# Kernel tuning notes

Measured on AMD Instinct MI355X. Metric: run time of the kernel, lower is better.

## Reference

```python
import jax, jax.numpy as jnp
import numpy as np

N, E, T = 8192, 131072, 12
H = 64        # node/edge/global hidden size
F = 1         # node_attr_size
OUT = 1       # out_size


def setup_inputs() -> dict:
    key = jax.random.key(0)
    ks = jax.random.split(key, 32)
    rn = lambda k, s, sc=1.0: jax.random.normal(k, s, dtype=jnp.float32) * sc
    w = 0.05  # weight scale
    inp = {
        "node_attrs": rn(ks[0], (T, N, F)),
        "edge_attrs": jax.random.uniform(ks[1], (T, E, 1), dtype=jnp.float32),
        "global_attr": rn(ks[2], (1, H)),
        "sp_L": rn(ks[3], (N, N), 0.01),
        "coeff": jax.random.uniform(ks[4], (1,), dtype=jnp.float32),
        # encoders
        "w_edge_enc": rn(ks[5], (H, 1), w), "b_edge_enc": jnp.zeros((H,), jnp.float32),
        "w_node_enc": rn(ks[6], (H, F), w), "b_node_enc": jnp.zeros((H,), jnp.float32),
        # block MLPs: in-dims from the Linear defs in __init__
        "w_eb": rn(ks[7], (H, (H + 2 * H) * 2 + H), w), "b_eb": jnp.zeros((H,), jnp.float32),
        "w_nb": rn(ks[8], (H, 2 * H + 2 * H + H), w), "b_nb": jnp.zeros((H,), jnp.float32),
        "w_gb": rn(ks[9], (H, H + H + H), w), "b_gb": jnp.zeros((H,), jnp.float32),
        # GRU (1 layer, input F, hidden H) + output head
        "gru_w_ih": rn(ks[10], (3 * H, F), w), "gru_w_hh": rn(ks[11], (3 * H, H), w),
        "gru_b_ih": jnp.zeros((3 * H,), jnp.float32), "gru_b_hh": jnp.zeros((3 * H,), jnp.float32),
        "w_lout": rn(ks[12], (OUT, H), w), "b_lout": jnp.zeros((OUT,), jnp.float32),
        "edge_index": jax.random.randint(ks[13], (2, E), 0, N),
        "num_processing_steps": T,
    }
    return inp


def _forward(node_attrs, edge_attrs, global_attr, sp_L, coeff,
             w_edge_enc, b_edge_enc, w_node_enc, b_node_enc,
             w_eb, b_eb, w_nb, b_nb, w_gb, b_gb,
             gru_w_ih, gru_w_hh, gru_b_ih, gru_b_hh,
             w_lout, b_lout, edge_index):
    n_nodes = node_attrs.shape[1]
    n_edges = edge_attrs.shape[1]
    send, recv = edge_index[0], edge_index[1]

    # encoders (edge_enc / node_enc), applied per time step
    enc_e = jax.nn.relu(jnp.einsum('tef,hf->teh', edge_attrs, w_edge_enc) + b_edge_enc)  # [T,E,H]
    enc_n = jax.nn.relu(jnp.einsum('tnf,hf->tnh', node_attrs, w_node_enc) + b_node_enc)  # [T,N,H]

    # per-node GRU over the T-step scalar history (torch nn.GRU math)
    def gru_step(h, x_t):  # h [N,H], x_t [N,F]
        gx = x_t @ gru_w_ih.T + gru_b_ih   # [N,3H]
        gh = h @ gru_w_hh.T + gru_b_hh     # [N,3H]
        xr, xz, xn = jnp.split(gx, 3, axis=-1)
        hr, hz, hn = jnp.split(gh, 3, axis=-1)
        r = jax.nn.sigmoid(xr + hr)
        z = jax.nn.sigmoid(xz + hz)
        n = jnp.tanh(xn + r * hn)
        return (1.0 - z) * n + z * h, None

    h0 = jnp.zeros((n_nodes, gru_w_hh.shape[1]), node_attrs.dtype)
    hT, _ = jax.lax.scan(gru_step, h0, node_attrs)          # [N,H]
    his = hT @ w_lout.T + b_lout                            # [N,OUT] == nodes_attr_based_on_his

    # GN layer 1: recurrent hidden graph (h_init zeros), per-step edge/node/global blocks
    def gn_step(carry, xs):
        hx, he, gl = carry          # hidden node [N,H], hidden edge [E,H], global [1,H]
        nx, ee = xs                 # encoded node [N,H], encoded edge [E,H]
        gl_e = jnp.broadcast_to(gl, (n_edges, gl.shape[1]))
        e_in = jnp.concatenate([ee, nx[send], nx[recv], he, hx[send], hx[recv], gl_e], axis=-1)
        new_e = jax.nn.relu(e_in @ w_eb.T + b_eb)           # [E,H]
        sent = jax.ops.segment_sum(new_e, send, num_segments=n_nodes)   # scatter_add by sender
        recvd = jax.ops.segment_sum(new_e, recv, num_segments=n_nodes)  # scatter_add by receiver
        gl_n = jnp.broadcast_to(gl, (n_nodes, gl.shape[1]))
        n_in = jnp.concatenate([nx, hx, recvd, sent, gl_n], axis=-1)
        new_n = jax.nn.relu(n_in @ w_nb.T + b_nb)           # [N,H]
        g_in = jnp.concatenate([new_n.mean(0, keepdims=True),
                                new_e.mean(0, keepdims=True), gl], axis=-1)
        new_g = jax.nn.relu(g_in @ w_gb.T + b_gb)           # [1,H]
        sd = coeff[0] * (sp_L @ new_n)                      # spatial derivative (pde='diff')
        td = new_n - hx                                     # time derivative of hidden state
        return (new_n, new_e, new_g), (td, sd)

    hx0 = jnp.zeros_like(enc_n[0])
    he0 = jnp.zeros_like(enc_e[0])
    _, (tds, sds) = jax.lax.scan(gn_step, (hx0, he0, global_attr), (enc_n, enc_e))

    pred_result = his[None]  # skip=True path: pred = nodes_attr_based_on_his.unsqueeze(0)
    return pred_result, tds, sds


def reference(node_attrs, edge_attrs, global_attr, sp_L, coeff,
              w_edge_enc, b_edge_enc, w_node_enc, b_node_enc,
              w_eb, b_eb, w_nb, b_nb, w_gb, b_gb,
              gru_w_ih, gru_w_hh, gru_b_ih, gru_b_hh,
              w_lout, b_lout, edge_index, num_processing_steps):
    del num_processing_steps  # fixed to leading dim of node_attrs
    return _forward(node_attrs, edge_attrs, global_attr, sp_L, coeff,
                    w_edge_enc, b_edge_enc, w_node_enc, b_node_enc,
                    w_eb, b_eb, w_nb, b_nb, w_gb, b_gb,
                    gru_w_ih, gru_w_hh, gru_b_ih, gru_b_hh,
                    w_lout, b_lout, edge_index)
```

## Files before the change

### kernel.cpp

```cpp
#include <hip/hip_runtime.h>
#include <math.h>

#define NN 8192
#define NE 131072
#define TT 12

typedef __attribute__((ext_vector_type(8))) short bf16x8;
typedef __attribute__((ext_vector_type(4))) float f32x4;

static const size_t OFF_HX    = 0;
static const size_t OFF_HE0   = OFF_HX    + (size_t)NN*64;
static const size_t OFF_HE1   = OFF_HE0   + (size_t)NE*64;
static const size_t OFF_A25   = OFF_HE1   + (size_t)NE*64;
static const size_t OFF_A36   = OFF_A25   + (size_t)NN*64;
static const size_t OFF_SENT  = OFF_A36   + (size_t)NN*64;
static const size_t OFF_RECVD = OFF_SENT  + (size_t)NN*64;
static const size_t OFF_NEWN  = OFF_RECVD + (size_t)NN*64;
static const size_t OFF_GL    = OFF_NEWN  + (size_t)NN*TT*32;
static const size_t OFF_CBE   = OFF_GL    + 64;
static const size_t OFF_CBN   = OFF_CBE   + 64;
static const size_t OFF_ESUM  = OFF_CBN   + 64;
static const size_t OFF_NSUM  = OFF_ESUM  + 64;
static const size_t OFF_EBF   = OFF_NSUM  + 64;

__device__ inline unsigned short f2bf(float x) {
  union { float f; unsigned u; } v; v.f = x;
  unsigned r = v.u + 0x7fffu + ((v.u >> 16) & 1u);
  return (unsigned short)(r >> 16);
}
__device__ inline float bf2f(unsigned short h) {
  union { unsigned u; float f; } v; v.u = ((unsigned)h) << 16;
  return v.f;
}
__device__ inline void split8(const float* x, bf16x8& hi, bf16x8& lo) {
  #pragma unroll
  for (int j = 0; j < 8; ++j) {
    unsigned short h = f2bf(x[j]);
    hi[j] = (short)h;
    lo[j] = (short)f2bf(x[j] - bf2f(h));
  }
}

__global__ void init_kernel(float* __restrict__ ws, const float* __restrict__ global_attr) {
  size_t total = (size_t)NN*64 + (size_t)NE*64;
  for (size_t i = (size_t)blockIdx.x*blockDim.x + threadIdx.x; i < total;
       i += (size_t)gridDim.x*blockDim.x)
    ws[OFF_HX + i] = 0.f;
  if (blockIdx.x == 0 && threadIdx.x < 64)
    ws[OFF_GL + threadIdx.x] = global_attr[threadIdx.x];
}

__global__ void prep_kernel(const float* __restrict__ w_eb, const float* __restrict__ b_eb,
                            const float* __restrict__ w_nb, const float* __restrict__ b_nb,
                            float* __restrict__ ws) {
  int h = threadIdx.x;
  float se = b_eb[h], sn = b_nb[h];
  for (int c = 0; c < 64; ++c) {
    float g = ws[OFF_GL + c];
    se += w_eb[h*448 + 384 + c] * g;
    sn += w_nb[h*320 + 256 + c] * g;
  }
  ws[OFF_CBE + h] = se;
  ws[OFF_CBN + h] = sn;
  ws[OFF_ESUM + h] = 0.f;
  ws[OFF_NSUM + h] = 0.f;
}

__global__ void ebfrag_kernel(const float* __restrict__ w_eb, unsigned short* __restrict__ ebf) {
  int idx = blockIdx.x*256 + threadIdx.x;
  if (idx >= 24576) return;
  int s = idx >> 12;
  int rem = idx & 4095;
  int k = rem >> 6;
  int n = rem & 63;
  float w = (s < 3) ? w_eb[n*448 + k] : w_eb[n*448 + 192 + k];
  unsigned short h = f2bf(w);
  unsigned short l = f2bf(w - bf2f(h));
  unsigned short val = (s == 2 || s == 5) ? l : h;
  int kh = k >> 5, q = (k >> 3) & 3, j = k & 7;
  int nt = n >> 4, col = n & 15;
  int lane = q*16 + col;
  ebf[(((size_t)(s*2 + kh)*4 + nt)*64 + lane)*8 + j] = val;
}

__global__ __launch_bounds__(256) void gru_his_kernel(
    const float* __restrict__ node_attrs, const float* __restrict__ w_ih,
    const float* __restrict__ w_hh, const float* __restrict__ b_ih,
    const float* __restrict__ b_hh, const float* __restrict__ w_lout,
    const float* __restrict__ b_lout, float* __restrict__ pred_out)
{
  __shared__ float Whh[192*65];
  __shared__ float wih_s[192], bih_s[192], bhh_s[192], wlo_s[64];
  int tid = threadIdx.x;
  for (int i = tid; i < 192*64; i += 256) {
    int rr = i >> 6, k = i & 63;
    Whh[rr*65 + k] = w_hh[i];
  }
  for (int i = tid; i < 192; i += 256) { wih_s[i] = w_ih[i]; bih_s[i] = b_ih[i]; bhh_s[i] = b_hh[i]; }
  if (tid < 64) wlo_s[tid] = w_lout[tid];
  __syncthreads();
  int lane = tid & 63, wv = tid >> 6;
  int n = blockIdx.x*4 + wv;
  int j = lane;
  float h = 0.f;
  for (int t = 0; t < TT; ++t) {
    float x = node_attrs[t*NN + n];
    float ar = 0.f, az = 0.f, an = 0.f;
    #pragma unroll 16
    for (int k = 0; k < 64; ++k) {
      float hk = __shfl(h, k);
      ar += hk * Whh[j*65 + k];
      az += hk * Whh[(64+j)*65 + k];
      an += hk * Whh[(128+j)*65 + k];
    }
    float xr = x*wih_s[j]      + bih_s[j];
    float xz = x*wih_s[64+j]   + bih_s[64+j];
    float xn = x*wih_s[128+j]  + bih_s[128+j];
    float r  = 1.f/(1.f + expf(-(xr + ar + bhh_s[j])));
    float z  = 1.f/(1.f + expf(-(xz + az + bhh_s[64+j])));
    float nnv = tanhf(xn + r*(an + bhh_s[128+j]));
    h = (1.f - z)*nnv + z*h;
  }
  float v = h * wlo_s[j];
  #pragma unroll
  for (int off = 32; off >= 1; off >>= 1) v += __shfl_xor(v, off);
  if (lane == 0) pred_out[n] = v + b_lout[0];
}

__global__ __launch_bounds__(256) void node_proj_kernel(
    const float* __restrict__ node_attrs, const float* __restrict__ w_eb,
    const float* __restrict__ w_node_enc, const float* __restrict__ b_node_enc,
    float* __restrict__ ws, int t)
{
  __shared__ float W2[64*65], W3[64*65], W5[64*65], W6[64*65];
  __shared__ float wne[64], bne[64];
  int tid = threadIdx.x;
  for (int i = tid; i < 64*64; i += 256) {
    int h = i >> 6, c = i & 63;
    W2[h*65+c] = w_eb[h*448 + 64  + c];
    W3[h*65+c] = w_eb[h*448 + 128 + c];
    W5[h*65+c] = w_eb[h*448 + 256 + c];
    W6[h*65+c] = w_eb[h*448 + 320 + c];
  }
  if (tid < 64) { wne[tid] = w_node_enc[tid]; bne[tid] = b_node_enc[tid]; }
  __syncthreads();
  int lane = tid & 63, wv = tid >> 6;
  float* A25 = ws + OFF_A25; float* A36 = ws + OFF_A36;
  float* hx = ws + OFF_HX;
  float* sent = ws + OFF_SENT; float* recvd = ws + OFF_RECVD;
  for (int q = 0; q < 4; ++q) {
    int n = blockIdx.x*16 + wv*4 + q;
    float na = node_attrs[t*NN + n];
    float nx = fmaxf(na*wne[lane] + bne[lane], 0.f);
    float hv = hx[n*64 + lane];
    float a2 = 0.f, a3 = 0.f, a5 = 0.f, a6 = 0.f;
    #pragma unroll 16
    for (int c = 0; c < 64; ++c) {
      float nxc = __shfl(nx, c);
      float hvc = __shfl(hv, c);
      int wi = lane*65 + c;
      a2 += W2[wi]*nxc; a3 += W3[wi]*nxc;
      a5 += W5[wi]*hvc; a6 += W6[wi]*hvc;
    }
    A25[n*64+lane] = a2 + a5; A36[n*64+lane] = a3 + a6;
    sent[n*64+lane] = 0.f; recvd[n*64+lane] = 0.f;
  }
}

__global__ __launch_bounds__(256) void edge_mfma_kernel(
    const float* __restrict__ edge_attrs, const int* __restrict__ edge_index,
    const float* __restrict__ w_edge_enc, const float* __restrict__ b_edge_enc,
    const unsigned short* __restrict__ ebf, float* __restrict__ ws,
    const float* __restrict__ he_cur, float* __restrict__ he_next, int t)
{
  __shared__ unsigned short Bs[12*4*64*8];
  __shared__ float wee_s[64], bee_s[64], cbe_s[64];
  __shared__ float esum_s[64];
  int tid = threadIdx.x;
  for (int i = tid; i < 3072; i += 256)
    ((uint4*)Bs)[i] = ((const uint4*)ebf)[i];
  if (tid < 64) { wee_s[tid]=w_edge_enc[tid]; bee_s[tid]=b_edge_enc[tid]; cbe_s[tid]=ws[OFF_CBE+tid]; esum_s[tid]=0.f; }
  __syncthreads();
  int lane = tid & 63, wv = tid >> 6;
  int m = lane & 15, q = lane >> 4;
  int e0 = blockIdx.x * 64;
  int em = e0 + wv*16 + m;
  float ea = edge_attrs[(size_t)t*NE + em];
  bf16x8 eeH[2], eeL[2], heH[2], heL[2];
  #pragma unroll
  for (int kh = 0; kh < 2; ++kh) {
    float xs[8];
    #pragma unroll
    for (int j = 0; j < 8; ++j) {
      int c = kh*32 + q*8 + j;
      xs[j] = fmaxf(ea*wee_s[c] + bee_s[c], 0.f);
    }
    split8(xs, eeH[kh], eeL[kh]);
    float4 h0 = *(const float4*)(he_cur + (size_t)em*64 + kh*32 + q*8);
    float4 h1 = *(const float4*)(he_cur + (size_t)em*64 + kh*32 + q*8 + 4);
    float hs[8] = {h0.x,h0.y,h0.z,h0.w,h1.x,h1.y,h1.z,h1.w};
    split8(hs, heH[kh], heL[kh]);
  }
  f32x4 acc[4] = {};
  #pragma unroll
  for (int s = 0; s < 6; ++s) {
    #pragma unroll
    for (int kh = 0; kh < 2; ++kh) {
      bf16x8 a = (s==0||s==2) ? eeH[kh] : (s==1) ? eeL[kh] : (s==4) ? heL[kh] : heH[kh];
      const bf16x8* bp = (const bf16x8*)(Bs + (size_t)((s*2+kh)*4*64)*8);
      #pragma unroll
      for (int nt = 0; nt < 4; ++nt) {
        bf16x8 b = bp[nt*64 + lane];
        acc[nt] = __builtin_amdgcn_mfma_f32_16x16x32_bf16(a, b, acc[nt], 0, 0, 0);
      }
    }
  }
  const int* sendi = edge_index;
  const int* recvi = edge_index + NE;
  const float* A25 = ws + OFF_A25;
  const float* A36 = ws + OFF_A36;
  float* sent = ws + OFF_SENT; float* recvd = ws + OFF_RECVD;
  int col = lane & 15;
  float part[4] = {0.f, 0.f, 0.f, 0.f};
  #pragma unroll
  for (int r = 0; r < 4; ++r) {
    int e = e0 + wv*16 + q*4 + r;
    int se = sendi[e], re = recvi[e];
    #pragma unroll
    for (int nt = 0; nt < 4; ++nt) {
      int h = nt*16 + col;
      float v = acc[nt][r] + A25[(size_t)se*64 + h] + A36[(size_t)re*64 + h] + cbe_s[h];
      v = fmaxf(v, 0.f);
      he_next[(size_t)e*64 + h] = v;
      atomicAdd(&sent[(size_t)se*64 + h], v);
      atomicAdd(&recvd[(size_t)re*64 + h], v);
      part[nt] += v;
    }
  }
  #pragma unroll
  for (int nt = 0; nt < 4; ++nt) {
    part[nt] += __shfl_xor(part[nt], 16);
    part[nt] += __shfl_xor(part[nt], 32);
  }
  if (q == 0) {
    #pragma unroll
    for (int nt = 0; nt < 4; ++nt)
      atomicAdd(&esum_s[nt*16 + col], part[nt]);
  }
  __syncthreads();
  if (tid < 64) atomicAdd(&ws[OFF_ESUM + tid], esum_s[tid]);
}

__global__ __launch_bounds__(256) void node_kernel(
    const float* __restrict__ node_attrs, const float* __restrict__ w_nb,
    const float* __restrict__ w_node_enc, const float* __restrict__ b_node_enc,
    float* __restrict__ ws, float* __restrict__ tds_out, int t)
{
  __shared__ float B1[64*65], B2[64*65], B3[64*65], B4[64*65];
  __shared__ float wne[64], bne[64], cbn[64];
  __shared__ float nsum_s[4][64];
  int tid = threadIdx.x;
  for (int i = tid; i < 64*64; i += 256) {
    int h = i >> 6, c = i & 63;
    B1[h*65+c] = w_nb[h*320 + c];
    B2[h*65+c] = w_nb[h*320 + 64  + c];
    B3[h*65+c] = w_nb[h*320 + 128 + c];
    B4[h*65+c] = w_nb[h*320 + 192 + c];
  }
  if (tid < 64) { wne[tid] = w_node_enc[tid]; bne[tid] = b_node_enc[tid]; cbn[tid] = ws[OFF_CBN + tid]; }
  __syncthreads();
  int lane = tid & 63, wv = tid >> 6;
  float* hx = ws + OFF_HX;
  const float* sent = ws + OFF_SENT; const float* recvd = ws + OFF_RECVD;
  unsigned short* newnT = (unsigned short*)(ws + OFF_NEWN);
  float npart = 0.f;
  for (int q = 0; q < 4; ++q) {
    int n = blockIdx.x*16 + wv*4 + q;
    float na = node_attrs[t*NN + n];
    float nx = fmaxf(na*wne[lane] + bne[lane], 0.f);
    float hv = hx[n*64 + lane];
    float rc = recvd[n*64 + lane];
    float st = sent[n*64 + lane];
    float acc = 0.f;
    #pragma unroll 16
    for (int c = 0; c < 64; ++c) {
      float nxc = __shfl(nx, c);
      float hvc = __shfl(hv, c);
      float rcc = __shfl(rc, c);
      float stc = __shfl(st, c);
      int wi = lane*65 + c;
      acc += B1[wi]*nxc + B2[wi]*hvc + B3[wi]*rcc + B4[wi]*stc;
    }
    acc += cbn[lane];
    float nn = fmaxf(acc, 0.f);
    tds_out[(size_t)t*NN*64 + (size_t)n*64 + lane] = nn - hv;
    hx[n*64 + lane] = nn;
    newnT[(size_t)(t*64 + lane)*NN + n] = f2bf(nn);
    npart += nn;
  }
  nsum_s[wv][lane] = npart;
  __syncthreads();
  if (tid < 64)
    atomicAdd(&ws[OFF_NSUM + tid],
              nsum_s[0][tid] + nsum_s[1][tid] + nsum_s[2][tid] + nsum_s[3][tid]);
}

__global__ void global_prep_kernel(
    const float* __restrict__ w_gb, const float* __restrict__ b_gb,
    const float* __restrict__ w_eb, const float* __restrict__ b_eb,
    const float* __restrict__ w_nb, const float* __restrict__ b_nb,
    float* __restrict__ ws)
{
  int h = threadIdx.x;
  __shared__ float gin[192];
  __shared__ float gs[64];
  gin[h]       = ws[OFF_NSUM + h] * (1.0f/NN);
  gin[64 + h]  = ws[OFF_ESUM + h] * (1.0f/NE);
  gin[128 + h] = ws[OFF_GL + h];
  __syncthreads();
  float a = b_gb[h];
  for (int c = 0; c < 192; ++c) a += w_gb[h*192 + c] * gin[c];
  float g = fmaxf(a, 0.f);
  gs[h] = g;
  __syncthreads();
  ws[OFF_GL + h] = g;
  float se = b_eb[h], sn = b_nb[h];
  for (int c = 0; c < 64; ++c) {
    float gc = gs[c];
    se += w_eb[h*448 + 384 + c] * gc;
    sn += w_nb[h*320 + 256 + c] * gc;
  }
  ws[OFF_CBE + h] = se;
  ws[OFF_CBN + h] = sn;
  ws[OFF_ESUM + h] = 0.f;
  ws[OFF_NSUM + h] = 0.f;
}

__global__ __launch_bounds__(512) void sds_mfma_kernel(
    const float* __restrict__ A, const unsigned short* __restrict__ Bt,
    float* __restrict__ P0, float* __restrict__ P1)
{
  __shared__ unsigned short Asm[2][64][72];
  int tid = threadIdx.x;
  int lane = tid & 63, wv = tid >> 6;
  int q = lane >> 4, l16 = lane & 15;
  int m0 = blockIdx.y * 64;
  int kbase = blockIdx.x * (NN/2);
  float* P = (blockIdx.x == 0) ? P0 : P1;

  int sr = tid >> 3;
  int sc = (tid & 7) * 8;
  const float* ap = A + (size_t)(m0 + sr)*NN + kbase + sc;

  const unsigned short* bp[6];
  #pragma unroll
  for (int ni = 0; ni < 6; ++ni)
    bp[ni] = Bt + (size_t)(wv*96 + ni*16 + l16)*NN + kbase + q*8;

  f32x4 acc[4][6] = {};

  {
    float4 a0 = *(const float4*)ap;
    float4 a1 = *(const float4*)(ap + 4);
    float xs[8] = {a0.x,a0.y,a0.z,a0.w,a1.x,a1.y,a1.z,a1.w};
    bf16x8 w;
    #pragma unroll
    for (int j = 0; j < 8; ++j) w[j] = (short)f2bf(xs[j]);
    *(bf16x8*)&Asm[0][sr][sc] = w;
  }

  const int NSLICE = (NN/2)/64;
  for (int ks = 0; ks < NSLICE; ++ks) {
    int buf = ks & 1;
    float4 a0, a1;
    if (ks + 1 < NSLICE) {
      a0 = *(const float4*)(ap + (ks+1)*64);
      a1 = *(const float4*)(ap + (ks+1)*64 + 4);
    }
    __syncthreads();
    #pragma unroll
    for (int sub = 0; sub < 2; ++sub) {
      bf16x8 bfr[6];
      #pragma unroll
      for (int ni = 0; ni < 6; ++ni)
        bfr[ni] = *(const bf16x8*)(bp[ni] + ks*64 + sub*32);
      bf16x8 af[4];
      #pragma unroll
      for (int mi = 0; mi < 4; ++mi)
        af[mi] = *(const bf16x8*)&Asm[buf][mi*16 + l16][sub*32 + q*8];
      #pragma unroll
      for (int mi = 0; mi < 4; ++mi)
        #pragma unroll
        for (int ni = 0; ni < 6; ++ni)
          acc[mi][ni] = __builtin_amdgcn_mfma_f32_16x16x32_bf16(af[mi], bfr[ni], acc[mi][ni], 0, 0, 0);
    }
    __syncthreads();
    if (ks + 1 < NSLICE) {
      float xs[8] = {a0.x,a0.y,a0.z,a0.w,a1.x,a1.y,a1.z,a1.w};
      bf16x8 w;
      #pragma unroll
      for (int j = 0; j < 8; ++j) w[j] = (short)f2bf(xs[j]);
      *(bf16x8*)&Asm[1-buf][sr][sc] = w;
    }
  }

  #pragma unroll
  for (int mi = 0; mi < 4; ++mi) {
    int row = m0 + mi*16 + q*4;
    #pragma unroll
    for (int ni = 0; ni < 6; ++ni) {
      int cn = wv*96 + ni*16 + l16;
      int tt = cn >> 6, h = cn & 63;
      #pragma unroll
      for (int r = 0; r < 4; ++r)
        P[(size_t)tt*NN*64 + (size_t)(row + r)*64 + h] = acc[mi][ni][r];
    }
  }
}

__global__ __launch_bounds__(256) void sds_combine_kernel(
    const float* __restrict__ P0, const float* __restrict__ P1,
    float* __restrict__ C, const float* __restrict__ coeff)
{
  float cf = coeff[0];
  size_t total = (size_t)TT*NN*64/4;
  for (size_t i = (size_t)blockIdx.x*blockDim.x + threadIdx.x; i < total;
       i += (size_t)gridDim.x*blockDim.x) {
    float4 p0 = ((const float4*)P0)[i];
    float4 p1 = ((const float4*)P1)[i];
    float4 c;
    c.x = cf*(p0.x + p1.x); c.y = cf*(p0.y + p1.y);
    c.z = cf*(p0.z + p1.z); c.w = cf*(p0.w + p1.w);
    ((float4*)C)[i] = c;
  }
}

extern "C" void kernel_launch(void* const* d_in, const int* in_sizes, int n_in,
                              void* d_out, int out_size, void* d_ws, size_t ws_size,
                              hipStream_t stream) {
  const float* node_attrs  = (const float*)d_in[0];
  const float* edge_attrs  = (const float*)d_in[1];
  const float* global_attr = (const float*)d_in[2];
  const float* sp_L        = (const float*)d_in[3];
  const float* coeff       = (const float*)d_in[4];
  const float* w_edge_enc  = (const float*)d_in[5];
  const float* b_edge_enc  = (const float*)d_in[6];
  const float* w_node_enc  = (const float*)d_in[7];
  const float* b_node_enc  = (const float*)d_in[8];
  const float* w_eb        = (const float*)d_in[9];
  const float* b_eb        = (const float*)d_in[10];
  const float* w_nb        = (const float*)d_in[11];
  const float* b_nb        = (const float*)d_in[12];
  const float* w_gb        = (const float*)d_in[13];
  const float* b_gb        = (const float*)d_in[14];
  const float* gru_w_ih    = (const float*)d_in[15];
  const float* gru_w_hh    = (const float*)d_in[16];
  const float* gru_b_ih    = (const float*)d_in[17];
  const float* gru_b_hh    = (const float*)d_in[18];
  const float* w_lout      = (const float*)d_in[19];
  const float* b_lout      = (const float*)d_in[20];
  const int*   edge_index  = (const int*)d_in[21];

  float* ws  = (float*)d_ws;
  float* out = (float*)d_out;
  float* pred_out = out;
  float* tds_out  = out + NN;
  float* sds_out  = tds_out + (size_t)TT*NN*64;
  unsigned short* ebf = (unsigned short*)(ws + OFF_EBF);

  hipLaunchKernelGGL(init_kernel, dim3(1024), dim3(256), 0, stream, ws, global_attr);
  hipLaunchKernelGGL(ebfrag_kernel, dim3(96), dim3(256), 0, stream, w_eb, ebf);
  hipLaunchKernelGGL(gru_his_kernel, dim3(NN/4), dim3(256), 0, stream,
                     node_attrs, gru_w_ih, gru_w_hh, gru_b_ih, gru_b_hh,
                     w_lout, b_lout, pred_out);
  hipLaunchKernelGGL(prep_kernel, dim3(1), dim3(64), 0, stream, w_eb, b_eb, w_nb, b_nb, ws);

  for (int t = 0; t < TT; ++t) {
    float* he_cur  = ws + ((t & 1) ? OFF_HE1 : OFF_HE0);
    float* he_next = ws + ((t & 1) ? OFF_HE0 : OFF_HE1);
    hipLaunchKernelGGL(node_proj_kernel, dim3(NN/16), dim3(256), 0, stream,
                       node_attrs, w_eb, w_node_enc, b_node_enc, ws, t);
    hipLaunchKernelGGL(edge_mfma_kernel, dim3(NE/64), dim3(256), 0, stream,
                       edge_attrs, edge_index, w_edge_enc, b_edge_enc,
                       ebf, ws, he_cur, he_next, t);
    hipLaunchKernelGGL(node_kernel, dim3(NN/16), dim3(256), 0, stream,
                       node_attrs, w_nb, w_node_enc, b_node_enc, ws, tds_out, t);
    hipLaunchKernelGGL(global_prep_kernel, dim3(1), dim3(64), 0, stream,
                       w_gb, b_gb, w_eb, b_eb, w_nb, b_nb, ws);
  }

  hipLaunchKernelGGL(sds_mfma_kernel, dim3(2, NN/64), dim3(512), 0, stream,
                     sp_L, (const unsigned short*)(ws + OFF_NEWN),
                     ws + OFF_HE0, ws + OFF_HE1);
  hipLaunchKernelGGL(sds_combine_kernel, dim3(1536), dim3(256), 0, stream,
                     ws + OFF_HE0, ws + OFF_HE1, sds_out, coeff);
}
```

Measured before the change: 2.923 ms.

## Replace atomic scatter of edge messages with CSR gather in node kernel

Builds sender and receiver CSR indices once per call (histogram, scan, fill), then drops the per-edge float atomicAdds into sent/recvd. The node kernel now gathers the edge hidden states of each node's incident edges directly from he_next. This removes 2*E*64 atomics per step and the zeroing of the accumulators, at the cost of irregular gathers in the node kernel, extra setup kernels, and a single-block scan. Summation order also changes, so floating-point results are no longer order-nondeterministic but differ slightly from before.

Result: faster. 2.509 ms (-14.2%).

```diff
diff --git a/kernel.cpp b/kernel.cpp
--- a/kernel.cpp
+++ b/kernel.cpp
@@ -13,15 +13,15 @@
 static const size_t OFF_HE1   = OFF_HE0   + (size_t)NE*64;
 static const size_t OFF_A25   = OFF_HE1   + (size_t)NE*64;
 static const size_t OFF_A36   = OFF_A25   + (size_t)NN*64;
-static const size_t OFF_SENT  = OFF_A36   + (size_t)NN*64;
-static const size_t OFF_RECVD = OFF_SENT  + (size_t)NN*64;
-static const size_t OFF_NEWN  = OFF_RECVD + (size_t)NN*64;
+static const size_t OFF_CSR   = OFF_A36   + (size_t)NN*64;
+static const size_t OFF_NEWN  = OFF_CSR   + (size_t)2*NN*64;
 static const size_t OFF_GL    = OFF_NEWN  + (size_t)NN*TT*32;
 static const size_t OFF_CBE   = OFF_GL    + 64;
 static const size_t OFF_CBN   = OFF_CBE   + 64;
 static const size_t OFF_ESUM  = OFF_CBN   + 64;
 static const size_t OFF_NSUM  = OFF_ESUM  + 64;
 static const size_t OFF_EBF   = OFF_NSUM  + 64;
+
 
 __device__ inline unsigned short f2bf(float x) {
   union { float f; unsigned u; } v; v.f = x;
@@ -64,6 +64,69 @@
   ws[OFF_CBN + h] = sn;
   ws[OFF_ESUM + h] = 0.f;
   ws[OFF_NSUM + h] = 0.f;
+}
+
+__global__ void csr_zero_kernel(int* __restrict__ ibase) {
+  int* cnt = ibase + 2*(NN+1);
+  int i = blockIdx.x*256 + threadIdx.x;
+  if (i < 2*NN) cnt[i] = 0;
+}
+
+__global__ void csr_hist_kernel(const int* __restrict__ ei, int* __restrict__ ibase) {
+  int* cnt_s = ibase + 2*(NN+1);
+  int* cnt_r = cnt_s + NN;
+  int e = blockIdx.x*256 + threadIdx.x;
+  if (e < NE) {
+    atomicAdd(&cnt_s[ei[e]], 1);
+    atomicAdd(&cnt_r[ei[NE + e]], 1);
+  }
+}
+
+__global__ __launch_bounds__(256) void csr_scan_kernel(int* __restrict__ ibase) {
+  __shared__ int part[257];
+  int tid = threadIdx.x;
+  int* ptr_s = ibase;
+  int* ptr_r = ibase + (NN+1);
+  int* cnt_s = ibase + 2*(NN+1);
+  int* cnt_r = cnt_s + NN;
+  for (int a = 0; a < 2; ++a) {
+    int* cnt = a ? cnt_r : cnt_s;
+    int* ptr = a ? ptr_r : ptr_s;
+    int loc[32];
+    int base = tid*32;
+    int s = 0;
+    #pragma unroll
+    for (int i = 0; i < 32; ++i) { loc[i] = s; s += cnt[base + i]; }
+    part[tid] = s;
+    __syncthreads();
+    if (tid == 0) {
+      int acc = 0;
+      for (int i = 0; i < 256; ++i) { int t = part[i]; part[i] = acc; acc += t; }
+      part[256] = acc;
+    }
+    __syncthreads();
+    int off = part[tid];
+    #pragma unroll
+    for (int i = 0; i < 32; ++i) {
+      int v = off + loc[i];
+      ptr[base + i] = v;
+      cnt[base + i] = v;
+    }
+    if (tid == 0) ptr[NN] = part[256];
+    __syncthreads();
+  }
+}
+
+__global__ void csr_fill_kernel(const int* __restrict__ ei, int* __restrict__ ibase) {
+  int* cnt_s = ibase + 2*(NN+1);
+  int* cnt_r = cnt_s + NN;
+  int* csr_s = cnt_r + NN;
+  int* csr_r = csr_s + NE;
+  int e = blockIdx.x*256 + threadIdx.x;
+  if (e < NE) {
+    int p = atomicAdd(&cnt_s[ei[e]], 1);      csr_s[p] = e;
+    int q = atomicAdd(&cnt_r[ei[NE + e]], 1); csr_r[q] = e;
+  }
 }
 
 __global__ void ebfrag_kernel(const float* __restrict__ w_eb, unsigned short* __restrict__ ebf) {
@@ -147,7 +210,6 @@
   int lane = tid & 63, wv = tid >> 6;
   float* A25 = ws + OFF_A25; float* A36 = ws + OFF_A36;
   float* hx = ws + OFF_HX;
-  float* sent = ws + OFF_SENT; float* recvd = ws + OFF_RECVD;
   for (int q = 0; q < 4; ++q) {
     int n = blockIdx.x*16 + wv*4 + q;
     float na = node_attrs[t*NN + n];
@@ -163,7 +225,6 @@
       a5 += W5[wi]*hvc; a6 += W6[wi]*hvc;
     }
     A25[n*64+lane] = a2 + a5; A36[n*64+lane] = a3 + a6;
-    sent[n*64+lane] = 0.f; recvd[n*64+lane] = 0.f;
   }
 }
 
@@ -219,7 +280,6 @@
   const int* recvi = edge_index + NE;
   const float* A25 = ws + OFF_A25;
   const float* A36 = ws + OFF_A36;
-  float* sent = ws + OFF_SENT; float* recvd = ws + OFF_RECVD;
   int col = lane & 15;
   float part[4] = {0.f, 0.f, 0.f, 0.f};
   #pragma unroll
@@ -232,8 +292,6 @@
       float v = acc[nt][r] + A25[(size_t)se*64 + h] + A36[(size_t)re*64 + h] + cbe_s[h];
       v = fmaxf(v, 0.f);
       he_next[(size_t)e*64 + h] = v;
-      atomicAdd(&sent[(size_t)se*64 + h], v);
-      atomicAdd(&recvd[(size_t)re*64 + h], v);
       part[nt] += v;
     }
   }
@@ -254,7 +312,8 @@
 __global__ __launch_bounds__(256) void node_kernel(
     const float* __restrict__ node_attrs, const float* __restrict__ w_nb,
     const float* __restrict__ w_node_enc, const float* __restrict__ b_node_enc,
-    float* __restrict__ ws, float* __restrict__ tds_out, int t)
+    float* __restrict__ ws, float* __restrict__ tds_out,
+    const float* __restrict__ he, int t)
 {
   __shared__ float B1[64*65], B2[64*65], B3[64*65], B4[64*65];
   __shared__ float wne[64], bne[64], cbn[64];
@@ -271,16 +330,40 @@
   __syncthreads();
   int lane = tid & 63, wv = tid >> 6;
   float* hx = ws + OFF_HX;
-  const float* sent = ws + OFF_SENT; const float* recvd = ws + OFF_RECVD;
+  const int* ibase = (const int*)(ws + OFF_CSR);
+  const int* ptr_s = ibase;
+  const int* ptr_r = ibase + (NN+1);
+  const int* csr_s = ibase + 2*(NN+1) + 2*NN;
+  const int* csr_r = csr_s + NE;
   unsigned short* newnT = (unsigned short*)(ws + OFF_NEWN);
   float npart = 0.f;
   for (int q = 0; q < 4; ++q) {
     int n = blockIdx.x*16 + wv*4 + q;
+    float st = 0.f;
+    {
+      int i = ptr_s[n], end = ptr_s[n+1];
+      for (; i + 4 <= end; i += 4) {
+        int e0 = csr_s[i], e1 = csr_s[i+1], e2 = csr_s[i+2], e3 = csr_s[i+3];
+        float v0 = he[(size_t)e0*64 + lane], v1 = he[(size_t)e1*64 + lane];
+        float v2 = he[(size_t)e2*64 + lane], v3 = he[(size_t)e3*64 + lane];
+        st += (v0 + v1) + (v2 + v3);
+      }
+      for (; i < end; ++i) st += he[(size_t)csr_s[i]*64 + lane];
+    }
+    float rc = 0.f;
+    {
+      int i = ptr_r[n], end = ptr_r[n+1];
+      for (; i + 4 <= end; i += 4) {
+        int e0 = csr_r[i], e1 = csr_r[i+1], e2 = csr_r[i+2], e3 = csr_r[i+3];
+        float v0 = he[(size_t)e0*64 + lane], v1 = he[(size_t)e1*64 + lane];
+        float v2 = he[(size_t)e2*64 + lane], v3 = he[(size_t)e3*64 + lane];
+        rc += (v0 + v1) + (v2 + v3);
+      }
+      for (; i < end; ++i) rc += he[(size_t)csr_r[i]*64 + lane];
+    }
     float na = node_attrs[t*NN + n];
     float nx = fmaxf(na*wne[lane] + bne[lane], 0.f);
     float hv = hx[n*64 + lane];
-    float rc = recvd[n*64 + lane];
-    float st = sent[n*64 + lane];
     float acc = 0.f;
     #pragma unroll 16
     for (int c = 0; c < 64; ++c) {
@@ -467,6 +550,7 @@
   float* tds_out  = out + NN;
   float* sds_out  = tds_out + (size_t)TT*NN*64;
   unsigned short* ebf = (unsigned short*)(ws + OFF_EBF);
+  int* ibase = (int*)(ws + OFF_CSR);
 
   hipLaunchKernelGGL(init_kernel, dim3(1024), dim3(256), 0, stream, ws, global_attr);
   hipLaunchKernelGGL(ebfrag_kernel, dim3(96), dim3(256), 0, stream, w_eb, ebf);
@@ -474,6 +558,11 @@
                      node_attrs, gru_w_ih, gru_w_hh, gru_b_ih, gru_b_hh,
                      w_lout, b_lout, pred_out);
   hipLaunchKernelGGL(prep_kernel, dim3(1), dim3(64), 0, stream, w_eb, b_eb, w_nb, b_nb, ws);
+
+  hipLaunchKernelGGL(csr_zero_kernel, dim3((2*NN+255)/256), dim3(256), 0, stream, ibase);
+  hipLaunchKernelGGL(csr_hist_kernel, dim3(NE/256), dim3(256), 0, stream, edge_index, ibase);
+  hipLaunchKernelGGL(csr_scan_kernel, dim3(1), dim3(256), 0, stream, ibase);
+  hipLaunchKernelGGL(csr_fill_kernel, dim3(NE/256), dim3(256), 0, stream, edge_index, ibase);
 
   for (int t = 0; t < TT; ++t) {
     float* he_cur  = ws + ((t & 1) ? OFF_HE1 : OFF_HE0);
@@ -484,7 +573,7 @@
                        edge_attrs, edge_index, w_edge_enc, b_edge_enc,
                        ebf, ws, he_cur, he_next, t);
     hipLaunchKernelGGL(node_kernel, dim3(NN/16), dim3(256), 0, stream,
-                       node_attrs, w_nb, w_node_enc, b_node_enc, ws, tds_out, t);
+                       node_attrs, w_nb, w_node_enc, b_node_enc, ws, tds_out, he_next, t);
     hipLaunchKernelGGL(global_prep_kernel, dim3(1), dim3(64), 0, stream,
                        w_gb, b_gb, w_eb, b_eb, w_nb, b_nb, ws);
   }
```
